# Kernel tuning notes

Measured on AMD Instinct MI355X. Metric: run time of the kernel, lower is better.

## Reference

```python
import jax, jax.numpy as jnp
import numpy as np

B, T, D, H = 64, 512, 512, 1024


def setup_inputs() -> dict:
    key = jax.random.key(0)
    k0, k1, k2, k3, k4 = jax.random.split(key, 5)
    s0 = 1.0 / np.sqrt(D + H)   # torch nn.Linear init bound, layer 0
    s1 = 1.0 / np.sqrt(H + H)   # layer 1
    x = jax.random.normal(k0, (B, T, D), jnp.float32)
    W0 = jax.random.uniform(k1, (4 * H, D + H), jnp.float32, -s0, s0)
    b0 = jax.random.uniform(k2, (4 * H,), jnp.float32, -s0, s0)
    W1 = jax.random.uniform(k3, (4 * H, H + H), jnp.float32, -s1, s1)
    b1 = jax.random.uniform(k4, (4 * H,), jnp.float32, -s1, s1)
    return {"x": x, "W0": W0, "b0": b0, "W1": W1, "b1": b1}


def _lstm_layer(x, W, b):
    # x: (B, T, Din); W: (4H, Din+H); b: (4H,)
    hdim = b.shape[0] // 4
    bsz = x.shape[0]
    h0 = jnp.zeros((bsz, hdim), x.dtype)
    c0 = jnp.zeros((bsz, hdim), x.dtype)

    def step(carry, x_t):
        h, c = carry
        z = jnp.concatenate([x_t, h], axis=-1) @ W.T + b  # (B, 4H)
        i, f, o, g = jnp.split(z, 4, axis=-1)             # torch split order i,f,o,g
        c_next = jax.nn.sigmoid(f) * c + jax.nn.sigmoid(i) * jnp.tanh(g)
        h_next = jax.nn.sigmoid(o) * jnp.tanh(c_next)
        return (h_next, c_next), h_next

    (_, _), hs = jax.lax.scan(step, (h0, c0), jnp.swapaxes(x, 0, 1))
    return jnp.swapaxes(hs, 0, 1)  # (B, T, H)


def reference(x, W0, b0, W1, b1):
    y = _lstm_layer(x, W0, b0)
    y = _lstm_layer(y, W1, b1)
    return y  # last layer output sequence (return_all_layers=False)
```

## Files before the change

### kernel.cpp

```cpp
#include <hip/hip_runtime.h>
#include <hip/hip_bf16.h>

typedef __bf16 bf16x8 __attribute__((ext_vector_type(8)));
typedef float  f32x4  __attribute__((ext_vector_type(4)));

#define MFMA16(a, b, c) __builtin_amdgcn_mfma_f32_16x16x32_bf16((a), (b), (c), 0, 0, 0)

static constexpr int Bz = 64, Tz = 512, Dz = 512, Hz = 1024;
static constexpr int NWG0 = 128;
static constexpr int NWGT = 256;
static constexpr int NJ   = 8;

static constexpr size_t LDS_BYTES = 131072;

static constexpr size_t N_W0X = 4096ull * 512;
static constexpr size_t N_W0H = 4096ull * 1024;
static constexpr size_t N_W1  = 4096ull * 2048;
static constexpr size_t N_Y0  = 64ull * 512 * 1024;
static constexpr size_t N_X   = 64ull * 512 * 512;
static constexpr size_t OFF_W0XH = 0;
static constexpr size_t OFF_W0XL = OFF_W0XH + N_W0X;
static constexpr size_t OFF_W0H  = OFF_W0XL + N_W0X;
static constexpr size_t OFF_W1   = OFF_W0H  + N_W0H;
static constexpr size_t OFF_Y0   = OFF_W1   + N_W1;
static constexpr size_t FLAGS_BYTE = (((OFF_Y0 + N_Y0) * 2) + 255) & ~(size_t)255;
static constexpr size_t H1S_BYTE   = FLAGS_BYTE + 4096;
static constexpr size_t WS_NEED    = H1S_BYTE + N_Y0 * 2;
static constexpr size_t XHI_BYTE   = H1S_BYTE + N_Y0 * 2;
static constexpr size_t XLO_BYTE   = XHI_BYTE + N_X * 2;
static constexpr size_t WS_NEED_X  = XLO_BYTE + N_X * 2;

static constexpr int STEP_ELEMS = 65536;

__device__ __forceinline__ float sigm(float x) { return 1.0f / (1.0f + __expf(-x)); }

__device__ __forceinline__ void st_agent_u32(void* p, unsigned v)
{ __hip_atomic_store((unsigned*)p, v, __ATOMIC_RELAXED, __HIP_MEMORY_SCOPE_AGENT); }
__device__ __forceinline__ void st_agent_f32(float* p, float v)
{ __hip_atomic_store(p, v, __ATOMIC_RELAXED, __HIP_MEMORY_SCOPE_AGENT); }

extern "C" __global__ void prep_split(const float* __restrict__ x,
                                      const float* __restrict__ W0,
                                      const float* __restrict__ W1,
                                      __bf16* __restrict__ ws,
                                      __bf16* __restrict__ xhi,
                                      __bf16* __restrict__ xlo)
{
    if (blockIdx.x == 0)
        for (int i = threadIdx.x; i < 1024; i += 256)
            ((unsigned*)((char*)ws + FLAGS_BYTE))[i] = 0u;

    __bf16* w0xh = ws + OFF_W0XH;
    __bf16* w0xl = ws + OFF_W0XL;
    __bf16* w0h  = ws + OFF_W0H;
    __bf16* w1c  = ws + OFF_W1;
    const size_t ntot = N_W0X + N_W0H + N_W1;
    const size_t stride = (size_t)gridDim.x * blockDim.x;
    for (size_t idx = (size_t)blockIdx.x * blockDim.x + threadIdx.x;
         idx < ntot; idx += stride) {
        if (idx < N_W0X) {
            size_t r = idx >> 9, c = idx & 511;
            float w = W0[r * 1536 + c];
            __bf16 hi = (__bf16)w;
            w0xh[idx] = hi;
            w0xl[idx] = (__bf16)(w - (float)hi);
        } else if (idx < N_W0X + N_W0H) {
            size_t i = idx - N_W0X;
            size_t r = i >> 10, c = i & 1023;
            w0h[i] = (__bf16)W0[r * 1536 + 512 + c];
        } else {
            size_t i = idx - N_W0X - N_W0H;
            w1c[i] = (__bf16)W1[i];
        }
    }
    if (xhi) {
        for (size_t idx = (size_t)blockIdx.x * blockDim.x + threadIdx.x;
             idx < N_X; idx += stride) {
            float v = x[idx];
            __bf16 hi = (__bf16)v;
            xhi[idx] = hi;
            xlo[idx] = (__bf16)(v - (float)hi);
        }
    }
}

__device__ __forceinline__ void publish(unsigned* p, unsigned v)
{
    asm volatile("s_waitcnt vmcnt(0)" ::: "memory");
    __hip_atomic_store(p, v, __ATOMIC_RELAXED, __HIP_MEMORY_SCOPE_AGENT);
}

__device__ __forceinline__ void wait_chunk32(const unsigned* flags, int base, unsigned target)
{
    const unsigned* p = flags + base + (threadIdx.x & 31);
    for (;;) {
        unsigned v = __hip_atomic_load(p, __ATOMIC_RELAXED, __HIP_MEMORY_SCOPE_AGENT);
        if (__all(v >= target)) break;
        __builtin_amdgcn_s_sleep(1);
    }
    asm volatile("" ::: "memory");
}

__device__ __forceinline__ void zx_ps(const __bf16* __restrict__ xh,
                                      const __bf16* __restrict__ xl,
    const __bf16* wxh0, const __bf16* wxl0,
    const __bf16* wxh1, const __bf16* wxl1,
    f32x4& zx0, f32x4& zx1)
{
    f32x4 a0 = {0,0,0,0}, a1 = {0,0,0,0};
#pragma unroll 4
    for (int kk = 0; kk < Dz / 32; ++kk) {
        bf16x8 ahi = *(const bf16x8*)(xh + kk * 32);
        bf16x8 alo = *(const bf16x8*)(xl + kk * 32);
        bf16x8 wh0 = *(const bf16x8*)(wxh0 + kk * 1024);
        bf16x8 wl0 = *(const bf16x8*)(wxl0 + kk * 1024);
        bf16x8 wh1 = *(const bf16x8*)(wxh1 + kk * 1024);
        bf16x8 wl1 = *(const bf16x8*)(wxl1 + kk * 1024);
        a0 = MFMA16(ahi, wh0, a0); a0 = MFMA16(alo, wh0, a0); a0 = MFMA16(ahi, wl0, a0);
        a1 = MFMA16(ahi, wh1, a1); a1 = MFMA16(alo, wh1, a1); a1 = MFMA16(ahi, wl1, a1);
    }
    zx0 = a0; zx1 = a1;
}

__device__ __forceinline__ void zx_fb(const float* __restrict__ xt,
    const __bf16* wxh0, const __bf16* wxl0,
    const __bf16* wxh1, const __bf16* wxl1,
    f32x4& zx0, f32x4& zx1)
{
    f32x4 a0 = {0,0,0,0}, a1 = {0,0,0,0};
#pragma unroll 4
    for (int kk = 0; kk < Dz / 32; ++kk) {
        f32x4 va = *(const f32x4*)(xt + kk * 32);
        f32x4 vb = *(const f32x4*)(xt + kk * 32 + 4);
        bf16x8 ahi, alo;
#pragma unroll
        for (int e = 0; e < 4; ++e) {
            float v = va[e]; __bf16 h1 = (__bf16)v;
            ahi[e] = h1; alo[e] = (__bf16)(v - (float)h1);
            float w = vb[e]; __bf16 h2 = (__bf16)w;
            ahi[4 + e] = h2; alo[4 + e] = (__bf16)(w - (float)h2);
        }
        bf16x8 wh0 = *(const bf16x8*)(wxh0 + kk * 1024);
        bf16x8 wl0 = *(const bf16x8*)(wxl0 + kk * 1024);
        bf16x8 wh1 = *(const bf16x8*)(wxh1 + kk * 1024);
        bf16x8 wl1 = *(const bf16x8*)(wxl1 + kk * 1024);
        a0 = MFMA16(ahi, wh0, a0); a0 = MFMA16(alo, wh0, a0); a0 = MFMA16(ahi, wl0, a0);
        a1 = MFMA16(ahi, wh1, a1); a1 = MFMA16(alo, wh1, a1); a1 = MFMA16(ahi, wl1, a1);
    }
    zx0 = a0; zx1 = a1;
}

template <bool F32OUT>
__device__ __forceinline__ void gates_store(
    f32x4 za, f32x4 zb, float* cs, int lane, int l15, int rowBase,
    unsigned* yline, float* yf32, size_t rowStride)
{
    f32x4 pa, pb;
#pragma unroll
    for (int e = 0; e < 4; ++e) { pa[e] = __shfl_xor(za[e], 8, 64); pb[e] = __shfl_xor(zb[e], 8, 64); }
    const bool hi = (l15 & 8) != 0;
    int p01[2];
#pragma unroll
    for (int k2 = 0; k2 < 2; ++k2) {
        float zi, zf, zo, zg;
        if (hi) { zi = pa[2 + k2]; zf = za[2 + k2]; zo = pb[2 + k2]; zg = zb[2 + k2]; }
        else    { zi = za[k2];     zf = pa[k2];     zo = zb[k2];     zg = pb[k2];     }
        float cn = sigm(zf) * cs[k2] + sigm(zi) * tanhf(zg);
        float hn = sigm(zo) * tanhf(cn);
        cs[k2] = cn;
        if (F32OUT) {
            int b = rowBase + (hi ? 2 : 0) + k2;
            st_agent_f32(&yf32[(size_t)b * rowStride], hn);
        }
        __bf16 hb = (__bf16)hn;
        unsigned bits = (unsigned)__builtin_bit_cast(unsigned short, hb);
        unsigned par  = __shfl_down(bits, 1, 64);
        p01[k2] = (int)(bits | (par << 16));
    }
    if (yline) {
        int r    = lane >> 2;
        int srcl = ((r >> 2) << 4) | (((r >> 1) & 1) << 3) | ((lane & 3) << 1);
        unsigned v0 = (unsigned)__builtin_amdgcn_ds_bpermute(srcl * 4, p01[0]);
        unsigned v1 = (unsigned)__builtin_amdgcn_ds_bpermute(srcl * 4, p01[1]);
        st_agent_u32(yline + lane, (r & 1) ? v1 : v0);
    }
}

__device__ __forceinline__ void layer0(
    const float* __restrict__ x,
    const __bf16* __restrict__ xhi, const __bf16* __restrict__ xlo,
    const __bf16* __restrict__ w0xh, const __bf16* __restrict__ w0xl,
    const __bf16* __restrict__ w0h,  const float* __restrict__ b0,
    __bf16* y0, __bf16* wtile, unsigned* flags0)
{
    const int tid  = threadIdx.x;
    const int wave = tid >> 6, lane = tid & 63, l15 = lane & 15, lg = lane >> 4;
    const int wg   = blockIdx.x;
    const int j0   = wg * NJ;

    __bf16* sWXH = wtile;
    __bf16* sWXL = wtile + 16384;
    __bf16* sWH  = wtile + 32768;
    for (int idx = tid; idx < 32 * (Dz / 8); idx += 256) {
        int r = idx >> 6, k8 = idx & 63;
        int kk = k8 >> 2, sub = k8 & 3;
        int dst = kk * 1024 + r * 32 + ((sub * 8) ^ (((r >> 2) & 3) * 8));
        size_t grow = (size_t)((r >> 3) * Hz + j0 + (r & 7));
        *(bf16x8*)(sWXH + dst) = *(const bf16x8*)(w0xh + grow * Dz + k8 * 8);
        *(bf16x8*)(sWXL + dst) = *(const bf16x8*)(w0xl + grow * Dz + k8 * 8);
    }
    for (int idx = tid; idx < 32 * (Hz / 8); idx += 256) {
        int r = idx >> 7, k8 = idx & 127;
        int kk = k8 >> 2, sub = k8 & 3;
        int dst = kk * 1024 + r * 32 + ((sub * 8) ^ (((r >> 2) & 3) * 8));
        size_t grow = (size_t)((r >> 3) * Hz + j0 + (r & 7));
        *(bf16x8*)(sWH + dst) = *(const bf16x8*)(w0h + grow * Hz + k8 * 8);
    }
    __syncthreads();

    const __bf16* wxh[2]; const __bf16* wxl[2]; const __bf16* whp[2]; float bv[2];
#pragma unroll
    for (int tn = 0; tn < 2; ++tn) {
        int c = tn * 16 + l15;
        int lofs = c * 32 + ((lg * 8) ^ (((c >> 2) & 3) * 8));
        wxh[tn] = sWXH + lofs;
        wxl[tn] = sWXL + lofs;
        whp[tn] = sWH  + lofs;
        bv[tn]  = b0[(c >> 3) * Hz + j0 + (c & 7)];
    }
    const int bA = wave * 16 + l15;
    const float*  xp  = x + (size_t)bA * Tz * Dz + lg * 8;
    const __bf16* xph = xhi ? xhi + (size_t)bA * Tz * Dz + lg * 8 : nullptr;
    const __bf16* xpl = xlo ? xlo + (size_t)bA * Tz * Dz + lg * 8 : nullptr;
    const __bf16* hp0 = y0 + wave * 128 + l15 * 8 + lg * 512;

    const unsigned* flw = flags0 + wave * 128;
    unsigned* myflag     = flags0 + wave * 128 + wg;

    float cs[2] = {0.f, 0.f};
    f32x4 zx0, zx1;
    if (xph) zx_ps(xph, xpl, wxh[0], wxl[0], wxh[1], wxl[1], zx0, zx1);
    else     zx_fb(xp,       wxh[0], wxl[0], wxh[1], wxl[1], zx0, zx1);

    for (int s = 0; s < Tz; ++s) {
        f32x4 ah0 = {0,0,0,0}, ah1 = {0,0,0,0};
        if (s > 0) {
            const __bf16* ht = hp0 + (size_t)(s - 1) * STEP_ELEMS;
            for (int c4 = 0; c4 < 4; ++c4) {
                wait_chunk32(flw, 32 * c4, (unsigned)s);
#pragma unroll
                for (int kk = 8 * c4; kk < 8 * c4 + 8; ++kk) {
                    bf16x8 a = *(const bf16x8*)(ht + kk * 2048);
                    ah0 = MFMA16(a, *(const bf16x8*)(whp[0] + kk * 1024), ah0);
                    ah1 = MFMA16(a, *(const bf16x8*)(whp[1] + kk * 1024), ah1);
                }
            }
        }
        f32x4 za, zb;
#pragma unroll
        for (int e = 0; e < 4; ++e) { za[e] = zx0[e] + ah0[e] + bv[0]; zb[e] = zx1[e] + ah1[e] + bv[1]; }

        unsigned* yline = (unsigned*)y0 + (size_t)s * (STEP_ELEMS / 2) + wg * 256 + wave * 64;
        gates_store<false>(za, zb, cs, lane, l15, wave * 16 + lg * 4, yline, nullptr, 0);

        publish(myflag, (unsigned)(s + 1));
        if (s < Tz - 1) {
            if (xph) zx_ps(xph + (size_t)(s + 1) * Dz, xpl + (size_t)(s + 1) * Dz,
                           wxh[0], wxl[0], wxh[1], wxl[1], zx0, zx1);
            else     zx_fb(xp + (size_t)(s + 1) * Dz,
                           wxh[0], wxl[0], wxh[1], wxl[1], zx0, zx1);
        }
    }
}

__device__ __forceinline__ void layer1(
    const __bf16* __restrict__ y0, const __bf16* __restrict__ w1c,
    const float* __restrict__ b1, float* out, __bf16* h1s,
    __bf16* wtile, unsigned* flags0, unsigned* flags1)
{
    const int tid  = threadIdx.x;
    const int wave = tid >> 6, lane = tid & 63, l15 = lane & 15, lg = lane >> 4;
    const int wg   = blockIdx.x - NWG0;
    const int j0   = wg * NJ;

    __bf16* sWX = wtile;
    __bf16* sWH = wtile + 32768;
    for (int idx = tid; idx < 32 * (Hz / 8); idx += 256) {
        int r = idx >> 7, k8 = idx & 127;
        int kk = k8 >> 2, sub = k8 & 3;
        int dst = kk * 1024 + r * 32 + ((sub * 8) ^ (((r >> 2) & 3) * 8));
        size_t grow = (size_t)((r >> 3) * Hz + j0 + (r & 7));
        const __bf16* srow = w1c + grow * 2048;
        *(bf16x8*)(sWX + dst) = *(const bf16x8*)(srow + k8 * 8);
        *(bf16x8*)(sWH + dst) = *(const bf16x8*)(srow + 1024 + k8 * 8);
    }
    __syncthreads();

    const __bf16* wxp[2]; const __bf16* whp[2]; float bv[2];
#pragma unroll
    for (int tn = 0; tn < 2; ++tn) {
        int c = tn * 16 + l15;
        int lofs = c * 32 + ((lg * 8) ^ (((c >> 2) & 3) * 8));
        wxp[tn] = sWX + lofs;
        whp[tn] = sWH + lofs;
        bv[tn]  = b1[(c >> 3) * Hz + j0 + (c & 7)];
    }
    const int bA = wave * 16 + l15;
    const __bf16* xp0 = y0 + wave * 128 + l15 * 8 + lg * 512;
    const float*  hpf = out + (size_t)bA * Tz * Hz + lg * 8;
    const __bf16* hs0 = h1s ? h1s + wave * 128 + l15 * 8 + lg * 512 : nullptr;

    const unsigned* fl0w = flags0 + wave * 128;
    const unsigned* fl1w = flags1 + wave * 128;
    unsigned* myflag      = flags1 + wave * 128 + wg;

    float cs[2] = {0.f, 0.f};

    for (int s = 1; s <= Tz; ++s) {
        const int t = s - 1;
        f32x4 ax0 = {bv[0], bv[0], bv[0], bv[0]};
        f32x4 ax1 = {bv[1], bv[1], bv[1], bv[1]};

        if (t > 0) {
            if (hs0) {
                const __bf16* ht = hs0 + (size_t)(t - 1) * STEP_ELEMS;
                for (int c4 = 0; c4 < 4; ++c4) {
                    wait_chunk32(fl1w, 32 * c4, (unsigned)(s - 1));
#pragma unroll
                    for (int kk = 8 * c4; kk < 8 * c4 + 8; ++kk) {
                        bf16x8 a = *(const bf16x8*)(ht + kk * 2048);
                        ax0 = MFMA16(a, *(const bf16x8*)(whp[0] + kk * 1024), ax0);
                        ax1 = MFMA16(a, *(const bf16x8*)(whp[1] + kk * 1024), ax1);
                    }
                }
            } else {
                const float* ht = hpf + (size_t)(t - 1) * Hz;
                for (int c4 = 0; c4 < 4; ++c4) {
                    wait_chunk32(fl1w, 32 * c4, (unsigned)(s - 1));
#pragma unroll
                    for (int kk = 8 * c4; kk < 8 * c4 + 8; ++kk) {
                        f32x4 va = *(const f32x4*)(ht + kk * 32);
                        f32x4 vb = *(const f32x4*)(ht + kk * 32 + 4);
                        bf16x8 a;
#pragma unroll
                        for (int e = 0; e < 4; ++e) { a[e] = (__bf16)va[e]; a[4 + e] = (__bf16)vb[e]; }
                        ax0 = MFMA16(a, *(const bf16x8*)(whp[0] + kk * 1024), ax0);
                        ax1 = MFMA16(a, *(const bf16x8*)(whp[1] + kk * 1024), ax1);
                    }
                }
            }
        }
        {
            const __bf16* xt = xp0 + (size_t)t * STEP_ELEMS;
            for (int c4 = 0; c4 < 4; ++c4) {
                wait_chunk32(fl0w, 32 * c4, (unsigned)s);
#pragma unroll
                for (int kk = 8 * c4; kk < 8 * c4 + 8; ++kk) {
                    bf16x8 a = *(const bf16x8*)(xt + kk * 2048);
                    ax0 = MFMA16(a, *(const bf16x8*)(wxp[0] + kk * 1024), ax0);
                    ax1 = MFMA16(a, *(const bf16x8*)(wxp[1] + kk * 1024), ax1);
                }
            }
        }

        unsigned* hline = h1s ? (unsigned*)h1s + (size_t)t * (STEP_ELEMS / 2) + wg * 256 + wave * 64
                              : nullptr;
        gates_store<true>(ax0, ax1, cs, lane, l15, wave * 16 + lg * 4,
                          hline, out + (size_t)t * Hz + j0 + (l15 & 7), (size_t)Tz * Hz);

        if (s < Tz) publish(myflag, (unsigned)s);
    }
}

extern "C" __global__ void __launch_bounds__(256, 1)
lstm2(const float* __restrict__ x,
      const float* __restrict__ b0,
      const float* __restrict__ b1,
      __bf16* ws,
      float* out,
      __bf16* h1s,
      const __bf16* __restrict__ xhi,
      const __bf16* __restrict__ xlo)
{
    extern __shared__ char lds_raw[];
    __bf16* wtile = (__bf16*)lds_raw;
    unsigned* flags0 = (unsigned*)((char*)ws + FLAGS_BYTE);
    unsigned* flags1 = (unsigned*)((char*)ws + FLAGS_BYTE + 2048);

    if (blockIdx.x < NWG0)
        layer0(x, xhi, xlo, ws + OFF_W0XH, ws + OFF_W0XL, ws + OFF_W0H, b0,
               ws + OFF_Y0, wtile, flags0);
    else
        layer1(ws + OFF_Y0, ws + OFF_W1, b1, out, h1s, wtile, flags0, flags1);
}

extern "C" void kernel_launch(void* const* d_in, const int* in_sizes, int n_in,
                              void* d_out, int out_size, void* d_ws, size_t ws_size,
                              hipStream_t stream)
{
    const float* x  = (const float*)d_in[0];
    const float* W0 = (const float*)d_in[1];
    const float* b0 = (const float*)d_in[2];
    const float* W1 = (const float*)d_in[3];
    const float* b1 = (const float*)d_in[4];
    float* out = (float*)d_out;
    __bf16* ws = (__bf16*)d_ws;
    __bf16* h1s = (ws_size >= WS_NEED)   ? (__bf16*)((char*)ws + H1S_BYTE) : nullptr;
    __bf16* xhi = (ws_size >= WS_NEED_X) ? (__bf16*)((char*)ws + XHI_BYTE) : nullptr;
    __bf16* xlo = (ws_size >= WS_NEED_X) ? (__bf16*)((char*)ws + XLO_BYTE) : nullptr;

    (void)hipFuncSetAttribute((const void*)lstm2,
                        hipFuncAttributeMaxDynamicSharedMemorySize, (int)LDS_BYTES);

    hipLaunchKernelGGL(prep_split, dim3(2048), dim3(256), 0, stream, x, W0, W1, ws, xhi, xlo);

    const __bf16* xhic = xhi; const __bf16* xloc = xlo;
    void* args[] = { (void*)&x, (void*)&b0, (void*)&b1, (void*)&ws, (void*)&out,
                     (void*)&h1s, (void*)&xhic, (void*)&xloc };
    (void)hipLaunchCooperativeKernel(reinterpret_cast<void*>(lstm2),
                               dim3(NWGT), dim3(256), args, LDS_BYTES, stream);
}
```

Baseline: 5.212 ms.

## Split K across waves with LDS reduction and per-workgroup step flags

Each wave previously computed the full K reduction for its own 16 batch rows. Now each wave handles a quarter of K for all four batch-row groups, and partial sums are reduced through an LDS scratch buffer. The flag protocol moves from one flag per wave to one flag per workgroup, written after a block barrier, so each wave only polls one chunk of producer flags. This is meant to shorten the per-step dependency chain and reduce flag polling. It adds an LDS round trip, extra LDS allocation and two block-wide barriers per timestep.

```diff
diff --git a/kernel.cpp b/kernel.cpp
--- a/kernel.cpp
+++ b/kernel.cpp
@@ -11,7 +11,9 @@
 static constexpr int NWGT = 256;
 static constexpr int NJ   = 8;
 
-static constexpr size_t LDS_BYTES = 131072;
+static constexpr size_t WT_BYTES  = 131072;
+static constexpr size_t ZACC_OFF  = WT_BYTES;
+static constexpr size_t LDS_BYTES = WT_BYTES + 24576;
 
 static constexpr size_t N_W0X = 4096ull * 512;
 static constexpr size_t N_W0H = 4096ull * 1024;
@@ -38,6 +40,8 @@
 { __hip_atomic_store((unsigned*)p, v, __ATOMIC_RELAXED, __HIP_MEMORY_SCOPE_AGENT); }
 __device__ __forceinline__ void st_agent_f32(float* p, float v)
 { __hip_atomic_store(p, v, __ATOMIC_RELAXED, __HIP_MEMORY_SCOPE_AGENT); }
+
+__device__ __forceinline__ int zslot(int k, int m) { return k * 3 + (m > k ? m - 1 : m); }
 
 extern "C" __global__ void prep_split(const float* __restrict__ x,
                                       const float* __restrict__ W0,
@@ -84,12 +88,6 @@
     }
 }
 
-__device__ __forceinline__ void publish(unsigned* p, unsigned v)
-{
-    asm volatile("s_waitcnt vmcnt(0)" ::: "memory");
-    __hip_atomic_store(p, v, __ATOMIC_RELAXED, __HIP_MEMORY_SCOPE_AGENT);
-}
-
 __device__ __forceinline__ void wait_chunk32(const unsigned* flags, int base, unsigned target)
 {
     const unsigned* p = flags + base + (threadIdx.x & 31);
@@ -101,53 +99,85 @@
     asm volatile("" ::: "memory");
 }
 
-__device__ __forceinline__ void zx_ps(const __bf16* __restrict__ xh,
-                                      const __bf16* __restrict__ xl,
-    const __bf16* wxh0, const __bf16* wxl0,
-    const __bf16* wxh1, const __bf16* wxl1,
-    f32x4& zx0, f32x4& zx1)
-{
-    f32x4 a0 = {0,0,0,0}, a1 = {0,0,0,0};
-#pragma unroll 4
-    for (int kk = 0; kk < Dz / 32; ++kk) {
-        bf16x8 ahi = *(const bf16x8*)(xh + kk * 32);
-        bf16x8 alo = *(const bf16x8*)(xl + kk * 32);
-        bf16x8 wh0 = *(const bf16x8*)(wxh0 + kk * 1024);
-        bf16x8 wl0 = *(const bf16x8*)(wxl0 + kk * 1024);
-        bf16x8 wh1 = *(const bf16x8*)(wxh1 + kk * 1024);
-        bf16x8 wl1 = *(const bf16x8*)(wxl1 + kk * 1024);
-        a0 = MFMA16(ahi, wh0, a0); a0 = MFMA16(alo, wh0, a0); a0 = MFMA16(ahi, wl0, a0);
-        a1 = MFMA16(ahi, wh1, a1); a1 = MFMA16(alo, wh1, a1); a1 = MFMA16(ahi, wl1, a1);
-    }
-    zx0 = a0; zx1 = a1;
-}
-
-__device__ __forceinline__ void zx_fb(const float* __restrict__ xt,
-    const __bf16* wxh0, const __bf16* wxl0,
-    const __bf16* wxh1, const __bf16* wxl1,
-    f32x4& zx0, f32x4& zx1)
-{
-    f32x4 a0 = {0,0,0,0}, a1 = {0,0,0,0};
-#pragma unroll 4
-    for (int kk = 0; kk < Dz / 32; ++kk) {
-        f32x4 va = *(const f32x4*)(xt + kk * 32);
-        f32x4 vb = *(const f32x4*)(xt + kk * 32 + 4);
-        bf16x8 ahi, alo;
-#pragma unroll
-        for (int e = 0; e < 4; ++e) {
-            float v = va[e]; __bf16 h1 = (__bf16)v;
-            ahi[e] = h1; alo[e] = (__bf16)(v - (float)h1);
-            float w = vb[e]; __bf16 h2 = (__bf16)w;
-            ahi[4 + e] = h2; alo[4 + e] = (__bf16)(w - (float)h2);
-        }
-        bf16x8 wh0 = *(const bf16x8*)(wxh0 + kk * 1024);
-        bf16x8 wl0 = *(const bf16x8*)(wxl0 + kk * 1024);
-        bf16x8 wh1 = *(const bf16x8*)(wxh1 + kk * 1024);
-        bf16x8 wl1 = *(const bf16x8*)(wxl1 + kk * 1024);
-        a0 = MFMA16(ahi, wh0, a0); a0 = MFMA16(alo, wh0, a0); a0 = MFMA16(ahi, wl0, a0);
-        a1 = MFMA16(ahi, wh1, a1); a1 = MFMA16(alo, wh1, a1); a1 = MFMA16(ahi, wl1, a1);
-    }
-    zx0 = a0; zx1 = a1;
+__device__ __forceinline__ void zxq_ps(f32x4 (&acc)[4][2], size_t tofs,
+    const __bf16* const (&xph)[4], const __bf16* const (&xpl)[4],
+    const __bf16* wxh0, const __bf16* wxl0, const __bf16* wxh1, const __bf16* wxl1)
+{
+#pragma unroll
+    for (int kkL = 0; kkL < 4; ++kkL) {
+        bf16x8 wh0 = *(const bf16x8*)(wxh0 + kkL * 1024);
+        bf16x8 wl0 = *(const bf16x8*)(wxl0 + kkL * 1024);
+        bf16x8 wh1 = *(const bf16x8*)(wxh1 + kkL * 1024);
+        bf16x8 wl1 = *(const bf16x8*)(wxl1 + kkL * 1024);
+#pragma unroll
+        for (int m = 0; m < 4; ++m) {
+            bf16x8 ahi = *(const bf16x8*)(xph[m] + tofs + kkL * 32);
+            bf16x8 alo = *(const bf16x8*)(xpl[m] + tofs + kkL * 32);
+            acc[m][0] = MFMA16(ahi, wh0, acc[m][0]);
+            acc[m][0] = MFMA16(alo, wh0, acc[m][0]);
+            acc[m][0] = MFMA16(ahi, wl0, acc[m][0]);
+            acc[m][1] = MFMA16(ahi, wh1, acc[m][1]);
+            acc[m][1] = MFMA16(alo, wh1, acc[m][1]);
+            acc[m][1] = MFMA16(ahi, wl1, acc[m][1]);
+        }
+    }
+}
+
+__device__ __forceinline__ void zxq_fb(f32x4 (&acc)[4][2], size_t tofs,
+    const float* const (&xpf)[4],
+    const __bf16* wxh0, const __bf16* wxl0, const __bf16* wxh1, const __bf16* wxl1)
+{
+#pragma unroll
+    for (int kkL = 0; kkL < 4; ++kkL) {
+        bf16x8 wh0 = *(const bf16x8*)(wxh0 + kkL * 1024);
+        bf16x8 wl0 = *(const bf16x8*)(wxl0 + kkL * 1024);
+        bf16x8 wh1 = *(const bf16x8*)(wxh1 + kkL * 1024);
+        bf16x8 wl1 = *(const bf16x8*)(wxl1 + kkL * 1024);
+#pragma unroll
+        for (int m = 0; m < 4; ++m) {
+            f32x4 va = *(const f32x4*)(xpf[m] + tofs + kkL * 32);
+            f32x4 vb = *(const f32x4*)(xpf[m] + tofs + kkL * 32 + 4);
+            bf16x8 ahi, alo;
+#pragma unroll
+            for (int e = 0; e < 4; ++e) {
+                float v = va[e]; __bf16 h1 = (__bf16)v;
+                ahi[e] = h1; alo[e] = (__bf16)(v - (float)h1);
+                float w = vb[e]; __bf16 h2 = (__bf16)w;
+                ahi[4 + e] = h2; alo[4 + e] = (__bf16)(w - (float)h2);
+            }
+            acc[m][0] = MFMA16(ahi, wh0, acc[m][0]);
+            acc[m][0] = MFMA16(alo, wh0, acc[m][0]);
+            acc[m][0] = MFMA16(ahi, wl0, acc[m][0]);
+            acc[m][1] = MFMA16(ahi, wh1, acc[m][1]);
+            acc[m][1] = MFMA16(alo, wh1, acc[m][1]);
+            acc[m][1] = MFMA16(ahi, wl1, acc[m][1]);
+        }
+    }
+}
+
+__device__ __forceinline__ void kreduce(f32x4 (&acc)[4][2], float* zacc,
+                                        int wave, int lane, const float* bv,
+                                        f32x4& za, f32x4& zb)
+{
+#pragma unroll
+    for (int m = 0; m < 4; ++m) {
+        if (m == wave) continue;
+        int sl = zslot(wave, m);
+        *(f32x4*)(zacc + ((sl * 2 + 0) * 64 + lane) * 4) = acc[m][0];
+        *(f32x4*)(zacc + ((sl * 2 + 1) * 64 + lane) * 4) = acc[m][1];
+    }
+    __syncthreads();
+    za = acc[wave][0];
+    zb = acc[wave][1];
+#pragma unroll
+    for (int k = 0; k < 4; ++k) {
+        if (k == wave) continue;
+        int sl = zslot(k, wave);
+        za += *(const f32x4*)(zacc + ((sl * 2 + 0) * 64 + lane) * 4);
+        zb += *(const f32x4*)(zacc + ((sl * 2 + 1) * 64 + lane) * 4);
+    }
+#pragma unroll
+    for (int e = 0; e < 4; ++e) { za[e] += bv[0]; zb[e] += bv[1]; }
 }
 
 template <bool F32OUT>
@@ -191,7 +221,7 @@
     const __bf16* __restrict__ xhi, const __bf16* __restrict__ xlo,
     const __bf16* __restrict__ w0xh, const __bf16* __restrict__ w0xl,
     const __bf16* __restrict__ w0h,  const float* __restrict__ b0,
-    __bf16* y0, __bf16* wtile, unsigned* flags0)
+    __bf16* y0, __bf16* wtile, float* zacc, unsigned* flags0)
 {
     const int tid  = threadIdx.x;
     const int wave = tid >> 6, lane = tid & 63, l15 = lane & 15, lg = lane >> 4;
@@ -223,52 +253,61 @@
     for (int tn = 0; tn < 2; ++tn) {
         int c = tn * 16 + l15;
         int lofs = c * 32 + ((lg * 8) ^ (((c >> 2) & 3) * 8));
-        wxh[tn] = sWXH + lofs;
-        wxl[tn] = sWXL + lofs;
-        whp[tn] = sWH  + lofs;
+        wxh[tn] = sWXH + lofs + wave * 4096;
+        wxl[tn] = sWXL + lofs + wave * 4096;
+        whp[tn] = sWH  + lofs + wave * 8192;
         bv[tn]  = b0[(c >> 3) * Hz + j0 + (c & 7)];
     }
-    const int bA = wave * 16 + l15;
-    const float*  xp  = x + (size_t)bA * Tz * Dz + lg * 8;
-    const __bf16* xph = xhi ? xhi + (size_t)bA * Tz * Dz + lg * 8 : nullptr;
-    const __bf16* xpl = xlo ? xlo + (size_t)bA * Tz * Dz + lg * 8 : nullptr;
-    const __bf16* hp0 = y0 + wave * 128 + l15 * 8 + lg * 512;
-
-    const unsigned* flw = flags0 + wave * 128;
-    unsigned* myflag     = flags0 + wave * 128 + wg;
-
+    const __bf16* xph[4]; const __bf16* xpl[4]; const float* xpf[4]; const __bf16* hpm[4];
+#pragma unroll
+    for (int m = 0; m < 4; ++m) {
+        size_t rofs = (size_t)(m * 16 + l15) * Tz * Dz + wave * 128 + lg * 8;
+        xph[m] = xhi ? xhi + rofs : nullptr;
+        xpl[m] = xlo ? xlo + rofs : nullptr;
+        xpf[m] = x + rofs;
+        hpm[m] = y0 + m * 128 + l15 * 8 + lg * 512 + wave * 8 * 2048;
+    }
+
+    unsigned* myflag = flags0 + wg;
     float cs[2] = {0.f, 0.f};
-    f32x4 zx0, zx1;
-    if (xph) zx_ps(xph, xpl, wxh[0], wxl[0], wxh[1], wxl[1], zx0, zx1);
-    else     zx_fb(xp,       wxh[0], wxl[0], wxh[1], wxl[1], zx0, zx1);
+
+    f32x4 acc[4][2];
+#pragma unroll
+    for (int m = 0; m < 4; ++m) { acc[m][0] = f32x4{0,0,0,0}; acc[m][1] = f32x4{0,0,0,0}; }
+    if (xhi) zxq_ps(acc, 0, xph, xpl, wxh[0], wxl[0], wxh[1], wxl[1]);
+    else     zxq_fb(acc, 0, xpf,      wxh[0], wxl[0], wxh[1], wxl[1]);
 
     for (int s = 0; s < Tz; ++s) {
-        f32x4 ah0 = {0,0,0,0}, ah1 = {0,0,0,0};
         if (s > 0) {
-            const __bf16* ht = hp0 + (size_t)(s - 1) * STEP_ELEMS;
-            for (int c4 = 0; c4 < 4; ++c4) {
-                wait_chunk32(flw, 32 * c4, (unsigned)s);
-#pragma unroll
-                for (int kk = 8 * c4; kk < 8 * c4 + 8; ++kk) {
-                    bf16x8 a = *(const bf16x8*)(ht + kk * 2048);
-                    ah0 = MFMA16(a, *(const bf16x8*)(whp[0] + kk * 1024), ah0);
-                    ah1 = MFMA16(a, *(const bf16x8*)(whp[1] + kk * 1024), ah1);
+            wait_chunk32(flags0, 32 * wave, (unsigned)s);
+            const size_t hofs = (size_t)(s - 1) * STEP_ELEMS;
+#pragma unroll
+            for (int kkL = 0; kkL < 8; ++kkL) {
+                bf16x8 w0v = *(const bf16x8*)(whp[0] + kkL * 1024);
+                bf16x8 w1v = *(const bf16x8*)(whp[1] + kkL * 1024);
+#pragma unroll
+                for (int m = 0; m < 4; ++m) {
+                    bf16x8 a = *(const bf16x8*)(hpm[m] + hofs + kkL * 2048);
+                    acc[m][0] = MFMA16(a, w0v, acc[m][0]);
+                    acc[m][1] = MFMA16(a, w1v, acc[m][1]);
                 }
             }
         }
         f32x4 za, zb;
-#pragma unroll
-        for (int e = 0; e < 4; ++e) { za[e] = zx0[e] + ah0[e] + bv[0]; zb[e] = zx1[e] + ah1[e] + bv[1]; }
+        kreduce(acc, zacc, wave, lane, bv, za, zb);
 
         unsigned* yline = (unsigned*)y0 + (size_t)s * (STEP_ELEMS / 2) + wg * 256 + wave * 64;
         gates_store<false>(za, zb, cs, lane, l15, wave * 16 + lg * 4, yline, nullptr, 0);
 
-        publish(myflag, (unsigned)(s + 1));
+        asm volatile("s_waitcnt vmcnt(0)" ::: "memory");
+        __syncthreads();
+        if (tid == 0) st_agent_u32(myflag, (unsigned)(s + 1));
+
         if (s < Tz - 1) {
-            if (xph) zx_ps(xph + (size_t)(s + 1) * Dz, xpl + (size_t)(s + 1) * Dz,
-                           wxh[0], wxl[0], wxh[1], wxl[1], zx0, zx1);
-            else     zx_fb(xp + (size_t)(s + 1) * Dz,
-                           wxh[0], wxl[0], wxh[1], wxl[1], zx0, zx1);
+#pragma unroll
+            for (int m = 0; m < 4; ++m) { acc[m][0] = f32x4{0,0,0,0}; acc[m][1] = f32x4{0,0,0,0}; }
+            if (xhi) zxq_ps(acc, (size_t)(s + 1) * Dz, xph, xpl, wxh[0], wxl[0], wxh[1], wxl[1]);
+            else     zxq_fb(acc, (size_t)(s + 1) * Dz, xpf,      wxh[0], wxl[0], wxh[1], wxl[1]);
         }
     }
 }
@@ -276,7 +315,7 @@
 __device__ __forceinline__ void layer1(
     const __bf16* __restrict__ y0, const __bf16* __restrict__ w1c,
     const float* __restrict__ b1, float* out, __bf16* h1s,
-    __bf16* wtile, unsigned* flags0, unsigned* flags1)
+    __bf16* wtile, float* zacc, unsigned* flags0, unsigned* flags1)
 {
     const int tid  = threadIdx.x;
     const int wave = tid >> 6, lane = tid & 63, l15 = lane & 15, lg = lane >> 4;
@@ -301,74 +340,88 @@
     for (int tn = 0; tn < 2; ++tn) {
         int c = tn * 16 + l15;
         int lofs = c * 32 + ((lg * 8) ^ (((c >> 2) & 3) * 8));
-        wxp[tn] = sWX + lofs;
-        whp[tn] = sWH + lofs;
+        wxp[tn] = sWX + lofs + wave * 8192;
+        whp[tn] = sWH + lofs + wave * 8192;
         bv[tn]  = b1[(c >> 3) * Hz + j0 + (c & 7)];
     }
-    const int bA = wave * 16 + l15;
-    const __bf16* xp0 = y0 + wave * 128 + l15 * 8 + lg * 512;
-    const float*  hpf = out + (size_t)bA * Tz * Hz + lg * 8;
-    const __bf16* hs0 = h1s ? h1s + wave * 128 + l15 * 8 + lg * 512 : nullptr;
-
-    const unsigned* fl0w = flags0 + wave * 128;
-    const unsigned* fl1w = flags1 + wave * 128;
-    unsigned* myflag      = flags1 + wave * 128 + wg;
-
+    const __bf16* xp0[4]; const __bf16* hs0[4]; const float* hpf[4];
+#pragma unroll
+    for (int m = 0; m < 4; ++m) {
+        xp0[m] = y0 + m * 128 + l15 * 8 + lg * 512 + wave * 8 * 2048;
+        hs0[m] = h1s ? h1s + m * 128 + l15 * 8 + lg * 512 + wave * 8 * 2048 : nullptr;
+        hpf[m] = out + (size_t)(m * 16 + l15) * Tz * Hz + lg * 8 + wave * 256;
+    }
+
+    unsigned* myflag = flags1 + wg;
     float cs[2] = {0.f, 0.f};
 
     for (int s = 1; s <= Tz; ++s) {
         const int t = s - 1;
-        f32x4 ax0 = {bv[0], bv[0], bv[0], bv[0]};
-        f32x4 ax1 = {bv[1], bv[1], bv[1], bv[1]};
+        f32x4 acc[4][2];
+#pragma unroll
+        for (int m = 0; m < 4; ++m) { acc[m][0] = f32x4{0,0,0,0}; acc[m][1] = f32x4{0,0,0,0}; }
 
         if (t > 0) {
-            if (hs0) {
-                const __bf16* ht = hs0 + (size_t)(t - 1) * STEP_ELEMS;
-                for (int c4 = 0; c4 < 4; ++c4) {
-                    wait_chunk32(fl1w, 32 * c4, (unsigned)(s - 1));
-#pragma unroll
-                    for (int kk = 8 * c4; kk < 8 * c4 + 8; ++kk) {
-                        bf16x8 a = *(const bf16x8*)(ht + kk * 2048);
-                        ax0 = MFMA16(a, *(const bf16x8*)(whp[0] + kk * 1024), ax0);
-                        ax1 = MFMA16(a, *(const bf16x8*)(whp[1] + kk * 1024), ax1);
+            wait_chunk32(flags1, 32 * wave, (unsigned)(s - 1));
+            if (h1s) {
+                const size_t hofs = (size_t)(t - 1) * STEP_ELEMS;
+#pragma unroll
+                for (int kkL = 0; kkL < 8; ++kkL) {
+                    bf16x8 w0v = *(const bf16x8*)(whp[0] + kkL * 1024);
+                    bf16x8 w1v = *(const bf16x8*)(whp[1] + kkL * 1024);
+#pragma unroll
+                    for (int m = 0; m < 4; ++m) {
+                        bf16x8 a = *(const bf16x8*)(hs0[m] + hofs + kkL * 2048);
+                        acc[m][0] = MFMA16(a, w0v, acc[m][0]);
+                        acc[m][1] = MFMA16(a, w1v, acc[m][1]);
                     }
                 }
             } else {
-                const float* ht = hpf + (size_t)(t - 1) * Hz;
-                for (int c4 = 0; c4 < 4; ++c4) {
-                    wait_chunk32(fl1w, 32 * c4, (unsigned)(s - 1));
-#pragma unroll
-                    for (int kk = 8 * c4; kk < 8 * c4 + 8; ++kk) {
-                        f32x4 va = *(const f32x4*)(ht + kk * 32);
-                        f32x4 vb = *(const f32x4*)(ht + kk * 32 + 4);
+                const size_t hofs = (size_t)(t - 1) * Hz;
+#pragma unroll
+                for (int kkL = 0; kkL < 8; ++kkL) {
+                    bf16x8 w0v = *(const bf16x8*)(whp[0] + kkL * 1024);
+                    bf16x8 w1v = *(const bf16x8*)(whp[1] + kkL * 1024);
+#pragma unroll
+                    for (int m = 0; m < 4; ++m) {
+                        f32x4 va = *(const f32x4*)(hpf[m] + hofs + kkL * 32);
+                        f32x4 vb = *(const f32x4*)(hpf[m] + hofs + kkL * 32 + 4);
                         bf16x8 a;
 #pragma unroll
                         for (int e = 0; e < 4; ++e) { a[e] = (__bf16)va[e]; a[4 + e] = (__bf16)vb[e]; }
-                        ax0 = MFMA16(a, *(const bf16x8*)(whp[0] + kk * 1024), ax0);
-                        ax1 = MFMA16(a, *(const bf16x8*)(whp[1] + kk * 1024), ax1);
+                        acc[m][0] = MFMA16(a, w0v, acc[m][0]);
+                        acc[m][1] = MFMA16(a, w1v, acc[m][1]);
                     }
                 }
             }
         }
         {
-            const __bf16* xt = xp0 + (size_t)t * STEP_ELEMS;
-            for (int c4 = 0; c4 < 4; ++c4) {
-                wait_chunk32(fl0w, 32 * c4, (unsigned)s);
-#pragma unroll
-                for (int kk = 8 * c4; kk < 8 * c4 + 8; ++kk) {
-                    bf16x8 a = *(const bf16x8*)(xt + kk * 2048);
-                    ax0 = MFMA16(a, *(const bf16x8*)(wxp[0] + kk * 1024), ax0);
-                    ax1 = MFMA16(a, *(const bf16x8*)(wxp[1] + kk * 1024), ax1);
+            wait_chunk32(flags0, 32 * wave, (unsigned)s);
+            const size_t xofs = (size_t)t * STEP_ELEMS;
+#pragma unroll
+            for (int kkL = 0; kkL < 8; ++kkL) {
+                bf16x8 w0v = *(const bf16x8*)(wxp[0] + kkL * 1024);
+                bf16x8 w1v = *(const bf16x8*)(wxp[1] + kkL * 1024);
+#pragma unroll
+                for (int m = 0; m < 4; ++m) {
+                    bf16x8 a = *(const bf16x8*)(xp0[m] + xofs + kkL * 2048);
+                    acc[m][0] = MFMA16(a, w0v, acc[m][0]);
+                    acc[m][1] = MFMA16(a, w1v, acc[m][1]);
                 }
             }
         }
 
+        f32x4 za, zb;
+        kreduce(acc, zacc, wave, lane, bv, za, zb);
+
         unsigned* hline = h1s ? (unsigned*)h1s + (size_t)t * (STEP_ELEMS / 2) + wg * 256 + wave * 64
                               : nullptr;
-        gates_store<true>(ax0, ax1, cs, lane, l15, wave * 16 + lg * 4,
+        gates_store<true>(za, zb, cs, lane, l15, wave * 16 + lg * 4,
                           hline, out + (size_t)t * Hz + j0 + (l15 & 7), (size_t)Tz * Hz);
 
-        if (s < Tz) publish(myflag, (unsigned)s);
+        asm volatile("s_waitcnt vmcnt(0)" ::: "memory");
+        __syncthreads();
+        if (tid == 0 && s < Tz) st_agent_u32(myflag, (unsigned)s);
     }
 }
 
@@ -384,14 +437,15 @@
 {
     extern __shared__ char lds_raw[];
     __bf16* wtile = (__bf16*)lds_raw;
+    float*  zacc  = (float*)(lds_raw + ZACC_OFF);
     unsigned* flags0 = (unsigned*)((char*)ws + FLAGS_BYTE);
     unsigned* flags1 = (unsigned*)((char*)ws + FLAGS_BYTE + 2048);
 
     if (blockIdx.x < NWG0)
         layer0(x, xhi, xlo, ws + OFF_W0XH, ws + OFF_W0XL, ws + OFF_W0H, b0,
-               ws + OFF_Y0, wtile, flags0);
+               ws + OFF_Y0, wtile, zacc, flags0);
     else
-        layer1(ws + OFF_Y0, ws + OFF_W1, b1, out, h1s, wtile, flags0, flags1);
+        layer1(ws + OFF_Y0, ws + OFF_W1, b1, out, h1s, wtile, zacc, flags0, flags1);
 }
 
 extern "C" void kernel_launch(void* const* d_in, const int* in_sizes, int n_in,
```

New measurement: 6.839 ms. 1.31x slower.
